# Kernel tuning notes

Measured on AMD Instinct MI355X. Metric: run time of the kernel, lower is better.

The kernel has to match this reference:

```python
import jax, jax.numpy as jnp
import numpy as np

B, I, H = 32768, 1024, 1024

def _xavier(key, shape):
    fan_out, fan_in = shape
    limit = float(np.sqrt(6.0 / (fan_in + fan_out)))
    return jax.random.uniform(key, shape, jnp.float32, -limit, limit)

def setup_inputs() -> dict:
    key = jax.random.key(0)
    ks = jax.random.split(key, 8)
    return {
        "x": jax.random.normal(ks[0], (B, I), jnp.float32),
        "h": jax.random.normal(ks[1], (B, H), jnp.float32),
        "weight_ir": _xavier(ks[2], (H, I)),
        "weight_hr": _xavier(ks[3], (H, H)),
        "weight_iz": _xavier(ks[4], (H, I)),
        "weight_hz": _xavier(ks[5], (H, H)),
        "weight_in": _xavier(ks[6], (H, I)),
        "weight_hn": _xavier(ks[7], (H, H)),
        "bias_ir": jnp.zeros((H,), jnp.float32),
        "bias_hr": jnp.zeros((H,), jnp.float32),
        "bias_iz": jnp.zeros((H,), jnp.float32),
        "bias_hz": jnp.zeros((H,), jnp.float32),
        "bias_in": jnp.zeros((H,), jnp.float32),
        "bias_hn": jnp.zeros((H,), jnp.float32),
    }

def reference(x, h, weight_ir, weight_hr, weight_iz, weight_hz, weight_in, weight_hn,
              bias_ir, bias_hr, bias_iz, bias_hz, bias_in, bias_hn):
    # Fuse the 3 input-side and 3 hidden-side GEMMs into two concatenated GEMMs
    # (same math as 6 separate F.linear calls).
    Wi = jnp.concatenate([weight_ir, weight_iz, weight_in], axis=0)  # [3H, I]
    Wh = jnp.concatenate([weight_hr, weight_hz, weight_hn], axis=0)  # [3H, H]
    bi = jnp.concatenate([bias_ir, bias_iz, bias_in])
    bh = jnp.concatenate([bias_hr, bias_hz, bias_hn])
    gi = x @ Wi.T + bi   # [B, 3H]
    gh = h @ Wh.T + bh   # [B, 3H]
    Hd = weight_hr.shape[0]
    ir, iz, inn = gi[:, :Hd], gi[:, Hd:2*Hd], gi[:, 2*Hd:]
    hr, hz, hn = gh[:, :Hd], gh[:, Hd:2*Hd], gh[:, 2*Hd:]
    r = jax.nn.sigmoid(ir + hr)
    z = jax.nn.sigmoid(iz + hz)
    n = jnp.tanh(inn + r * hn)
    return (1.0 - z) * n + z * h
```

## Files before the change

### kernel.cpp

```cpp
#include <hip/hip_runtime.h>
#include <hip/hip_bf16.h>


#define B_ROWS 32768
#define KD     1024
#define HD     1024

#define BM 128
#define BN 64
#define BK 32

typedef __bf16 bf16_t;
typedef __bf16 bf16x8 __attribute__((ext_vector_type(8)));
typedef __bf16 bf16x4 __attribute__((ext_vector_type(4)));
typedef float  f32x4  __attribute__((ext_vector_type(4)));

#define XT_BYTES  67108864ull
#define WT_OFF   134217728ull
#define WS_NEEDED 146800640ull

#define X_SLOTS 4194304
#define W_BASE_SLOT 8388608
#define TOTAL_SLOTS 9175040

__device__ __forceinline__ float sigm_f(float v) { return 1.0f / (1.0f + __expf(-v)); }
__device__ __forceinline__ float tanh_f(float v) { return 2.0f / (1.0f + __expf(-2.0f * v)) - 1.0f; }

__device__ __forceinline__ bf16x4 cvt4(f32x4 v) {
    bf16x4 r;
    r[0] = (bf16_t)v[0]; r[1] = (bf16_t)v[1];
    r[2] = (bf16_t)v[2]; r[3] = (bf16_t)v[3];
    return r;
}

__device__ __forceinline__ void glds16(const void* g, void* l) {
    __builtin_amdgcn_global_load_lds(
        (const __attribute__((address_space(1))) void*)g,
        (__attribute__((address_space(3))) void*)l, 16, 0, 0);
}

struct WPtrs { const float* p[6]; };

__global__ void __launch_bounds__(256)
cvt_kernel(const float* __restrict__ x, const float* __restrict__ h,
           WPtrs wp, bf16_t* __restrict__ ws)
{
    int sid = blockIdx.x * 256 + threadIdx.x;
    if (sid >= TOTAL_SLOTS) return;

    const float* src;
    if (sid < W_BASE_SLOT) {
        const float* base = (sid < X_SLOTS) ? x : h;
        int s2   = sid & (X_SLOTS - 1);
        int tile = s2 >> 9;
        int c    = s2 & 511;
        int row  = c >> 2, s = c & 3;
        int mt   = tile >> 5, kt = tile & 31;
        int ks   = s ^ ((row >> 1) & 3);
        src = base + (size_t)(mt * 128 + row) * KD + kt * 32 + ks * 8;
    } else {
        int s2   = sid - W_BASE_SLOT;
        int tile = s2 / 1536;
        int c    = s2 % 1536;
        int g    = c >> 8;
        int cc   = c & 255;
        int row  = cc >> 2, s = cc & 3;
        int nt   = tile >> 5, kt = tile & 31;
        int ks   = s ^ ((row >> 1) & 3);
        src = wp.p[g] + (size_t)(nt * 64 + row) * KD + kt * 32 + ks * 8;
    }
    f32x4 a = *(const f32x4*)src;
    f32x4 b = *(const f32x4*)(src + 4);
    bf16x8 o;
    o[0]=(bf16_t)a[0]; o[1]=(bf16_t)a[1]; o[2]=(bf16_t)a[2]; o[3]=(bf16_t)a[3];
    o[4]=(bf16_t)b[0]; o[5]=(bf16_t)b[1]; o[6]=(bf16_t)b[2]; o[7]=(bf16_t)b[3];
    *(bf16x8*)(ws + (size_t)sid * 8) = o;
}

__global__ void __launch_bounds__(256, 2)
gru_mfma_kernel(const bf16_t* __restrict__ xt, const bf16_t* __restrict__ ht,
                const bf16_t* __restrict__ wt,
                const float* __restrict__ h,
                const float* __restrict__ b_ir, const float* __restrict__ b_hr,
                const float* __restrict__ b_iz, const float* __restrict__ b_hz,
                const float* __restrict__ b_in, const float* __restrict__ b_hn,
                float* __restrict__ out)
{
    __shared__ __align__(16) char smem[2][40960];

    const int tid  = threadIdx.x;
    const int lane = tid & 63;
    const int wid  = tid >> 6;
    const int wr   = wid >> 1;
    const int wc   = wid & 1;

    const int nblk = HD / BN;
    const int bidN = blockIdx.x % nblk;
    const int bidM = blockIdx.x / nblk;
    const int rowBase = bidM * BM;
    const int colBase = bidN * BN;

    const char* xcb = (const char*)xt + (size_t)bidM * 32 * 8192;
    const char* hcb = (const char*)ht + (size_t)bidM * 32 * 8192;
    const char* wcb = (const char*)wt + (size_t)bidN * 32 * 24576;

    const f32x4 vzero = {0.f, 0.f, 0.f, 0.f};
    f32x4 accR[4][2], accZ[4][2], accIN[4][2], accHN[4][2];
    #pragma unroll
    for (int m = 0; m < 4; ++m)
        #pragma unroll
        for (int n = 0; n < 2; ++n) {
            accR[m][n] = vzero; accZ[m][n] = vzero;
            accIN[m][n] = vzero; accHN[m][n] = vzero;
        }

    const int fr  = lane & 15;
    const int sl  = lane >> 4;
    const int f   = (fr >> 1) & 3;
    const int col = ((sl ^ f) << 4);
    int aoff[4], boff[2];
    #pragma unroll
    for (int m = 0; m < 4; ++m) aoff[m] = (wr * 64 + m * 16 + fr) * 64 + col;
    #pragma unroll
    for (int n = 0; n < 2; ++n) boff[n] = (wc * 32 + n * 16 + fr) * 64 + col;

    auto STAGE = [&](int buf, int kt) {
        const char* xc  = xcb + (size_t)kt * 8192;
        const char* hc  = hcb + (size_t)kt * 8192;
        const char* wc2 = wcb + (size_t)kt * 24576;
        char* s = smem[buf];
        #pragma unroll
        for (int i = 0; i < 2; ++i) {
            int off = wid * 2048 + i * 1024;
            glds16(xc + off + lane * 16, s + off);
            glds16(hc + off + lane * 16, s + 8192 + off);
        }
        #pragma unroll
        for (int j = 0; j < 6; ++j) {
            int off = wid * 6144 + j * 1024;
            glds16(wc2 + off + lane * 16, s + 16384 + off);
        }
    };

    auto COMPUTE = [&](const char* s) {
        bf16x8 xa[4], ha[4];
        #pragma unroll
        for (int m = 0; m < 4; ++m) {
            xa[m] = *(const bf16x8*)(s + aoff[m]);
            ha[m] = *(const bf16x8*)(s + 8192 + aoff[m]);
        }
        bf16x8 wb[6][2];
        #pragma unroll
        for (int g = 0; g < 6; ++g)
            #pragma unroll
            for (int n = 0; n < 2; ++n)
                wb[g][n] = *(const bf16x8*)(s + 16384 + g * 4096 + boff[n]);

        #pragma unroll
        for (int m = 0; m < 4; ++m) {
            #pragma unroll
            for (int n = 0; n < 2; ++n) {
                accR[m][n]  = __builtin_amdgcn_mfma_f32_16x16x32_bf16(xa[m], wb[0][n], accR[m][n], 0, 0, 0);
                accR[m][n]  = __builtin_amdgcn_mfma_f32_16x16x32_bf16(ha[m], wb[1][n], accR[m][n], 0, 0, 0);
                accZ[m][n]  = __builtin_amdgcn_mfma_f32_16x16x32_bf16(xa[m], wb[2][n], accZ[m][n], 0, 0, 0);
                accZ[m][n]  = __builtin_amdgcn_mfma_f32_16x16x32_bf16(ha[m], wb[3][n], accZ[m][n], 0, 0, 0);
                accIN[m][n] = __builtin_amdgcn_mfma_f32_16x16x32_bf16(xa[m], wb[4][n], accIN[m][n], 0, 0, 0);
                accHN[m][n] = __builtin_amdgcn_mfma_f32_16x16x32_bf16(ha[m], wb[5][n], accHN[m][n], 0, 0, 0);
            }
        }
    };

    STAGE(0, 0);

    for (int kt = 0; kt < 31; ++kt) {
        STAGE((kt + 1) & 1, kt + 1);
        asm volatile("s_waitcnt vmcnt(10)" ::: "memory");
        __builtin_amdgcn_s_barrier();
        __builtin_amdgcn_sched_barrier(0);
        COMPUTE(smem[kt & 1]);
        __builtin_amdgcn_sched_barrier(0);
        __builtin_amdgcn_s_barrier();
    }
    asm volatile("s_waitcnt vmcnt(0)" ::: "memory");
    __builtin_amdgcn_s_barrier();
    __builtin_amdgcn_sched_barrier(0);
    COMPUTE(smem[1]);

    const int rq = (lane >> 4) * 4;
    float br[2], bz[2], bi[2], bh[2];
    #pragma unroll
    for (int n = 0; n < 2; ++n) {
        int c = colBase + wc * 32 + n * 16 + fr;
        br[n] = b_ir[c] + b_hr[c];
        bz[n] = b_iz[c] + b_hz[c];
        bi[n] = b_in[c];
        bh[n] = b_hn[c];
    }
    #pragma unroll
    for (int m = 0; m < 4; ++m) {
        #pragma unroll
        for (int n = 0; n < 2; ++n) {
            int gc = colBase + wc * 32 + n * 16 + fr;
            #pragma unroll
            for (int j = 0; j < 4; ++j) {
                int gr = rowBase + wr * 64 + m * 16 + rq + j;
                float rv = sigm_f(accR[m][n][j] + br[n]);
                float zv = sigm_f(accZ[m][n][j] + bz[n]);
                float nv = tanh_f(accIN[m][n][j] + bi[n] + rv * (accHN[m][n][j] + bh[n]));
                float hv = h[(size_t)gr * HD + gc];
                out[(size_t)gr * HD + gc] = (1.0f - zv) * nv + zv * hv;
            }
        }
    }
}

#define PK 40
__global__ void __launch_bounds__(256, 2)
gru_fused_kernel(const float* __restrict__ x,  const float* __restrict__ h,
                 const float* __restrict__ w_ir, const float* __restrict__ w_hr,
                 const float* __restrict__ w_iz, const float* __restrict__ w_hz,
                 const float* __restrict__ w_in, const float* __restrict__ w_hn,
                 const float* __restrict__ b_ir, const float* __restrict__ b_hr,
                 const float* __restrict__ b_iz, const float* __restrict__ b_hz,
                 const float* __restrict__ b_in, const float* __restrict__ b_hn,
                 float* __restrict__ out)
{
    __shared__ __align__(16) bf16_t xs[BM][PK];
    __shared__ __align__(16) bf16_t hs[BM][PK];
    __shared__ __align__(16) bf16_t ws[6][BN][PK];

    const int tid  = threadIdx.x;
    const int lane = tid & 63;
    const int wid  = tid >> 6;
    const int wr   = wid >> 1;
    const int wc   = wid & 1;

    const int nblk = HD / BN;
    const int bidN = blockIdx.x % nblk;
    const int bidM = blockIdx.x / nblk;
    const int rowBase = bidM * BM;
    const int colBase = bidN * BN;

    const float* wptr[6] = { w_ir, w_hr, w_iz, w_hz, w_in, w_hn };

    int sr[4], sc[4];
    #pragma unroll
    for (int i = 0; i < 4; ++i) {
        int idx = tid + i * 256;
        sr[i] = idx >> 3;
        sc[i] = (idx & 7) * 4;
    }
    int xoff[4];
    #pragma unroll
    for (int i = 0; i < 4; ++i) xoff[i] = (rowBase + sr[i]) * KD + sc[i];
    int woff[2];
    #pragma unroll
    for (int i = 0; i < 2; ++i) woff[i] = (colBase + sr[i]) * KD + sc[i];

    const f32x4 vzero = {0.f, 0.f, 0.f, 0.f};
    f32x4 accR[4][2], accZ[4][2], accIN[4][2], accHN[4][2];
    #pragma unroll
    for (int m = 0; m < 4; ++m)
        #pragma unroll
        for (int n = 0; n < 2; ++n) {
            accR[m][n] = vzero; accZ[m][n] = vzero;
            accIN[m][n] = vzero; accHN[m][n] = vzero;
        }

    const int fr = lane & 15;
    const int ko = (lane >> 4) * 8;

    for (int k0 = 0; k0 < KD; k0 += BK) {
        __syncthreads();
        #pragma unroll
        for (int i = 0; i < 4; ++i) {
            f32x4 vx = *(const f32x4*)&x[xoff[i] + k0];
            f32x4 vh = *(const f32x4*)&h[xoff[i] + k0];
            *(bf16x4*)&xs[sr[i]][sc[i]] = cvt4(vx);
            *(bf16x4*)&hs[sr[i]][sc[i]] = cvt4(vh);
        }
        #pragma unroll
        for (int g = 0; g < 6; ++g) {
            #pragma unroll
            for (int i = 0; i < 2; ++i) {
                f32x4 vw = *(const f32x4*)&wptr[g][woff[i] + k0];
                *(bf16x4*)&ws[g][sr[i]][sc[i]] = cvt4(vw);
            }
        }
        __syncthreads();

        bf16x8 xa[4], ha[4];
        #pragma unroll
        for (int m = 0; m < 4; ++m) {
            xa[m] = *(const bf16x8*)&xs[wr * 64 + m * 16 + fr][ko];
            ha[m] = *(const bf16x8*)&hs[wr * 64 + m * 16 + fr][ko];
        }
        bf16x8 wb[6][2];
        #pragma unroll
        for (int g = 0; g < 6; ++g)
            #pragma unroll
            for (int n = 0; n < 2; ++n)
                wb[g][n] = *(const bf16x8*)&ws[g][wc * 32 + n * 16 + fr][ko];

        #pragma unroll
        for (int m = 0; m < 4; ++m) {
            #pragma unroll
            for (int n = 0; n < 2; ++n) {
                accR[m][n]  = __builtin_amdgcn_mfma_f32_16x16x32_bf16(xa[m], wb[0][n], accR[m][n], 0, 0, 0);
                accR[m][n]  = __builtin_amdgcn_mfma_f32_16x16x32_bf16(ha[m], wb[1][n], accR[m][n], 0, 0, 0);
                accZ[m][n]  = __builtin_amdgcn_mfma_f32_16x16x32_bf16(xa[m], wb[2][n], accZ[m][n], 0, 0, 0);
                accZ[m][n]  = __builtin_amdgcn_mfma_f32_16x16x32_bf16(ha[m], wb[3][n], accZ[m][n], 0, 0, 0);
                accIN[m][n] = __builtin_amdgcn_mfma_f32_16x16x32_bf16(xa[m], wb[4][n], accIN[m][n], 0, 0, 0);
                accHN[m][n] = __builtin_amdgcn_mfma_f32_16x16x32_bf16(ha[m], wb[5][n], accHN[m][n], 0, 0, 0);
            }
        }
    }

    const int rq = (lane >> 4) * 4;
    float br[2], bz[2], bi[2], bh[2];
    #pragma unroll
    for (int n = 0; n < 2; ++n) {
        int c = colBase + wc * 32 + n * 16 + fr;
        br[n] = b_ir[c] + b_hr[c];
        bz[n] = b_iz[c] + b_hz[c];
        bi[n] = b_in[c];
        bh[n] = b_hn[c];
    }
    #pragma unroll
    for (int m = 0; m < 4; ++m) {
        #pragma unroll
        for (int n = 0; n < 2; ++n) {
            int gc = colBase + wc * 32 + n * 16 + fr;
            #pragma unroll
            for (int j = 0; j < 4; ++j) {
                int gr = rowBase + wr * 64 + m * 16 + rq + j;
                float rv = sigm_f(accR[m][n][j] + br[n]);
                float zv = sigm_f(accZ[m][n][j] + bz[n]);
                float nv = tanh_f(accIN[m][n][j] + bi[n] + rv * (accHN[m][n][j] + bh[n]));
                float hv = h[gr * HD + gc];
                out[gr * HD + gc] = (1.0f - zv) * nv + zv * hv;
            }
        }
    }
}

extern "C" void kernel_launch(void* const* d_in, const int* in_sizes, int n_in,
                              void* d_out, int out_size, void* d_ws, size_t ws_size,
                              hipStream_t stream) {
    const float* x    = (const float*)d_in[0];
    const float* h    = (const float*)d_in[1];
    const float* w_ir = (const float*)d_in[2];
    const float* w_hr = (const float*)d_in[3];
    const float* w_iz = (const float*)d_in[4];
    const float* w_hz = (const float*)d_in[5];
    const float* w_in = (const float*)d_in[6];
    const float* w_hn = (const float*)d_in[7];
    const float* b_ir = (const float*)d_in[8];
    const float* b_hr = (const float*)d_in[9];
    const float* b_iz = (const float*)d_in[10];
    const float* b_hz = (const float*)d_in[11];
    const float* b_in = (const float*)d_in[12];
    const float* b_hn = (const float*)d_in[13];
    float* out = (float*)d_out;

    if (ws_size >= WS_NEEDED) {
        bf16_t* ws = (bf16_t*)d_ws;
        WPtrs wp;
        wp.p[0] = w_ir; wp.p[1] = w_hr; wp.p[2] = w_iz;
        wp.p[3] = w_hz; wp.p[4] = w_in; wp.p[5] = w_hn;
        cvt_kernel<<<(TOTAL_SLOTS + 255) / 256, 256, 0, stream>>>(x, h, wp, ws);

        const bf16_t* xt = ws;
        const bf16_t* ht = ws + XT_BYTES / 2;
        const bf16_t* wt = ws + WT_OFF / 2;
        dim3 grid((B_ROWS / BM) * (HD / BN));
        gru_mfma_kernel<<<grid, 256, 0, stream>>>(
            xt, ht, wt, h, b_ir, b_hr, b_iz, b_hz, b_in, b_hn, out);
    } else {
        dim3 grid((B_ROWS / BM) * (HD / BN));
        gru_fused_kernel<<<grid, 256, 0, stream>>>(
            x, h, w_ir, w_hr, w_iz, w_hz, w_in, w_hn,
            b_ir, b_hr, b_iz, b_hz, b_in, b_hn, out);
    }
}
```

Before: 473.2 us.

## Double MFMA block tile to 256 rows with 512 threads sharing weight tiles

The MFMA GRU kernel now uses 256-row blocks of 8 waves (512 threads) instead of 128-row blocks of 4 waves. Each k-step's weight tile in shared memory is reused by twice as many rows, which halves weight global/L2 traffic per output. LDS per block grows to 2x56KB and launch bounds drop to one block per CU, so there are fewer resident waves to hide latency. The staging layout and waitcnt are adjusted to match, and the fallback kernel keeps its old tile sizes through new macros.

```diff
diff --git a/kernel.cpp b/kernel.cpp
--- a/kernel.cpp
+++ b/kernel.cpp
@@ -6,7 +6,7 @@
 #define KD     1024
 #define HD     1024
 
-#define BM 128
+#define BM 256
 #define BN 64
 #define BK 32
 
@@ -77,7 +77,7 @@
     *(bf16x8*)(ws + (size_t)sid * 8) = o;
 }
 
-__global__ void __launch_bounds__(256, 2)
+__global__ void __launch_bounds__(512, 1)
 gru_mfma_kernel(const bf16_t* __restrict__ xt, const bf16_t* __restrict__ ht,
                 const bf16_t* __restrict__ wt,
                 const float* __restrict__ h,
@@ -86,7 +86,7 @@
                 const float* __restrict__ b_in, const float* __restrict__ b_hn,
                 float* __restrict__ out)
 {
-    __shared__ __align__(16) char smem[2][40960];
+    __shared__ __align__(16) char smem[2][57344];
 
     const int tid  = threadIdx.x;
     const int lane = tid & 63;
@@ -100,8 +100,10 @@
     const int rowBase = bidM * BM;
     const int colBase = bidN * BN;
 
-    const char* xcb = (const char*)xt + (size_t)bidM * 32 * 8192;
-    const char* hcb = (const char*)ht + (size_t)bidM * 32 * 8192;
+    const char* x0 = (const char*)xt + (size_t)(2 * bidM)     * 32 * 8192;
+    const char* x1 = (const char*)xt + (size_t)(2 * bidM + 1) * 32 * 8192;
+    const char* h0 = (const char*)ht + (size_t)(2 * bidM)     * 32 * 8192;
+    const char* h1 = (const char*)ht + (size_t)(2 * bidM + 1) * 32 * 8192;
     const char* wcb = (const char*)wt + (size_t)bidN * 32 * 24576;
 
     const f32x4 vzero = {0.f, 0.f, 0.f, 0.f};
@@ -120,26 +122,28 @@
     const int col = ((sl ^ f) << 4);
     int aoff[4], boff[2];
     #pragma unroll
-    for (int m = 0; m < 4; ++m) aoff[m] = (wr * 64 + m * 16 + fr) * 64 + col;
-    #pragma unroll
-    for (int n = 0; n < 2; ++n) boff[n] = (wc * 32 + n * 16 + fr) * 64 + col;
+    for (int m = 0; m < 4; ++m) {
+        int rloc = (wr & 1) * 64 + m * 16 + fr;
+        aoff[m] = (wr >> 1) * 8192 + rloc * 64 + col;
+    }
+    #pragma unroll
+    for (int n = 0; n < 2; ++n) boff[n] = 32768 + (wc * 32 + n * 16 + fr) * 64 + col;
 
     auto STAGE = [&](int buf, int kt) {
-        const char* xc  = xcb + (size_t)kt * 8192;
-        const char* hc  = hcb + (size_t)kt * 8192;
-        const char* wc2 = wcb + (size_t)kt * 24576;
         char* s = smem[buf];
-        #pragma unroll
-        for (int i = 0; i < 2; ++i) {
-            int off = wid * 2048 + i * 1024;
-            glds16(xc + off + lane * 16, s + off);
-            glds16(hc + off + lane * 16, s + 8192 + off);
-        }
-        #pragma unroll
-        for (int j = 0; j < 6; ++j) {
-            int off = wid * 6144 + j * 1024;
-            glds16(wc2 + off + lane * 16, s + 16384 + off);
-        }
+        const char* xs_ = (wid < 4 ? x0 : x1) + (size_t)kt * 8192;
+        const char* hs_ = (wid < 4 ? h0 : h1) + (size_t)kt * 8192;
+        const int half = (wid >> 2) * 8192;
+        const int xo = (wid & 3) * 2048;
+        glds16(xs_ + xo + lane * 16,        s + half + xo);
+        glds16(xs_ + xo + 1024 + lane * 16, s + half + xo + 1024);
+        glds16(hs_ + xo + lane * 16,        s + 16384 + half + xo);
+        glds16(hs_ + xo + 1024 + lane * 16, s + 16384 + half + xo + 1024);
+        const char* wk = wcb + (size_t)kt * 24576;
+        const int wo = wid * 3072;
+        #pragma unroll
+        for (int j = 0; j < 3; ++j)
+            glds16(wk + wo + j * 1024 + lane * 16, s + 32768 + wo + j * 1024);
     };
 
     auto COMPUTE = [&](const char* s) {
@@ -147,14 +151,14 @@
         #pragma unroll
         for (int m = 0; m < 4; ++m) {
             xa[m] = *(const bf16x8*)(s + aoff[m]);
-            ha[m] = *(const bf16x8*)(s + 8192 + aoff[m]);
+            ha[m] = *(const bf16x8*)(s + 16384 + aoff[m]);
         }
         bf16x8 wb[6][2];
         #pragma unroll
         for (int g = 0; g < 6; ++g)
             #pragma unroll
             for (int n = 0; n < 2; ++n)
-                wb[g][n] = *(const bf16x8*)(s + 16384 + g * 4096 + boff[n]);
+                wb[g][n] = *(const bf16x8*)(s + g * 4096 + boff[n]);
 
         #pragma unroll
         for (int m = 0; m < 4; ++m) {
@@ -174,7 +178,7 @@
 
     for (int kt = 0; kt < 31; ++kt) {
         STAGE((kt + 1) & 1, kt + 1);
-        asm volatile("s_waitcnt vmcnt(10)" ::: "memory");
+        asm volatile("s_waitcnt vmcnt(7)" ::: "memory");
         __builtin_amdgcn_s_barrier();
         __builtin_amdgcn_sched_barrier(0);
         COMPUTE(smem[kt & 1]);
@@ -215,6 +219,8 @@
 }
 
 #define PK 40
+#define FBM 128
+#define FBN 64
 __global__ void __launch_bounds__(256, 2)
 gru_fused_kernel(const float* __restrict__ x,  const float* __restrict__ h,
                  const float* __restrict__ w_ir, const float* __restrict__ w_hr,
@@ -225,9 +231,9 @@
                  const float* __restrict__ b_in, const float* __restrict__ b_hn,
                  float* __restrict__ out)
 {
-    __shared__ __align__(16) bf16_t xs[BM][PK];
-    __shared__ __align__(16) bf16_t hs[BM][PK];
-    __shared__ __align__(16) bf16_t ws[6][BN][PK];
+    __shared__ __align__(16) bf16_t xs[FBM][PK];
+    __shared__ __align__(16) bf16_t hs[FBM][PK];
+    __shared__ __align__(16) bf16_t ws[6][FBN][PK];
 
     const int tid  = threadIdx.x;
     const int lane = tid & 63;
@@ -235,11 +241,11 @@
     const int wr   = wid >> 1;
     const int wc   = wid & 1;
 
-    const int nblk = HD / BN;
+    const int nblk = HD / FBN;
     const int bidN = blockIdx.x % nblk;
     const int bidM = blockIdx.x / nblk;
-    const int rowBase = bidM * BM;
-    const int colBase = bidN * BN;
+    const int rowBase = bidM * FBM;
+    const int colBase = bidN * FBN;
 
     const float* wptr[6] = { w_ir, w_hr, w_iz, w_hz, w_in, w_hn };
 
@@ -374,10 +380,10 @@
         const bf16_t* ht = ws + XT_BYTES / 2;
         const bf16_t* wt = ws + WT_OFF / 2;
         dim3 grid((B_ROWS / BM) * (HD / BN));
-        gru_mfma_kernel<<<grid, 256, 0, stream>>>(
+        gru_mfma_kernel<<<grid, 512, 0, stream>>>(
             xt, ht, wt, h, b_ir, b_hr, b_iz, b_hz, b_in, b_hn, out);
     } else {
-        dim3 grid((B_ROWS / BM) * (HD / BN));
+        dim3 grid((B_ROWS / FBM) * (HD / FBN));
         gru_fused_kernel<<<grid, 256, 0, stream>>>(
             x, h, w_ir, w_hr, w_iz, w_hz, w_in, w_hn,
             b_ir, b_hr, b_iz, b_hz, b_in, b_hn, out);
```

Result: slower. 539.0 us (+13.9%).
